# Performance work log

Hardware: AMD Instinct MI355X
Metric: run time of the kernel (lower is better)

## Reference

```python
import jax, jax.numpy as jnp
import numpy as np

N = 100000      # nodes
E = 1000000     # edges
IN = 128        # input features
H = 64          # hidden_channels
EPS = 1e-5      # BatchNorm eps


def _gcn_conv(x, W, b, src, dst, n):
    # PyG GCNConv: linear -> add self loops -> sym-norm -> scatter-add -> bias
    h = x @ W                                   # [n, H]
    loop = jnp.arange(n)
    s = jnp.concatenate([src, loop])            # [E+n]
    d = jnp.concatenate([dst, loop])
    deg = jax.ops.segment_sum(jnp.ones(s.shape, h.dtype), d, num_segments=n)
    dinv = jnp.where(deg > 0, jax.lax.rsqrt(deg), 0.0)
    norm = dinv[s] * dinv[d]                    # [E+n]
    out = jax.ops.segment_sum(h[s] * norm[:, None], d, num_segments=n)
    return out + b


def _bn_relu(x, gamma, beta):
    # BatchNorm1d, training-mode batch statistics (biased var), then ReLU
    m = x.mean(axis=0)
    v = x.var(axis=0)
    return jax.nn.relu((x - m) * jax.lax.rsqrt(v + EPS) * gamma + beta)


def setup_inputs() -> dict:
    key = jax.random.key(0)
    ks = jax.random.split(key, 10)
    x = jax.random.normal(ks[0], (N, IN), jnp.float32)
    edge_index = jax.random.randint(ks[1], (2, E), 0, N)
    W1 = jax.random.normal(ks[2], (IN, H), jnp.float32) / np.sqrt(IN)
    b1 = jnp.zeros((H,), jnp.float32)
    g1 = jnp.ones((H,), jnp.float32)
    bt1 = jnp.zeros((H,), jnp.float32)
    W2 = jax.random.normal(ks[3], (H, H), jnp.float32) / np.sqrt(H)
    b2 = jnp.zeros((H,), jnp.float32)
    g2 = jnp.ones((H,), jnp.float32)
    bt2 = jnp.zeros((H,), jnp.float32)
    return {"x": x, "edge_index": edge_index, "W1": W1, "b1": b1,
            "g1": g1, "bt1": bt1, "W2": W2, "b2": b2, "g2": g2, "bt2": bt2}


def reference(x, edge_index, W1, b1, g1, bt1, W2, b2, g2, bt2):
    src, dst = edge_index[0], edge_index[1]
    n = x.shape[0]
    h = _gcn_conv(x, W1, b1, src, dst, n)
    h = _bn_relu(h, g1, bt1)          # dropout omitted (deterministic reference)
    h = _gcn_conv(h, W2, b2, src, dst, n)
    h = _bn_relu(h, g2, bt2)
    return h
```

## Files before the change

### kernel.cpp

```cpp
#include <hip/hip_runtime.h>


#define IN_F 128
#define HID  64
#define SLOTS 64
static constexpr float BN_EPS = 1e-5f;

typedef float f32x4 __attribute__((ext_vector_type(4)));
typedef short bf16x8 __attribute__((ext_vector_type(8)));

__device__ inline unsigned short f2bf(float f) {
    union { float f; unsigned u; } v; v.f = f;
    unsigned r = v.u + 0x7FFFu + ((v.u >> 16) & 1u);
    return (unsigned short)(r >> 16);
}
__device__ inline float bf2f(unsigned short h) {
    union { unsigned u; float f; } v; v.u = (unsigned)h << 16;
    return v.f;
}


__global__ void fill_slots_convw(const int* __restrict__ src, const int* __restrict__ dst,
                                 int* __restrict__ cnt, int* __restrict__ slots, int E,
                                 const float* __restrict__ W1, const float* __restrict__ W2,
                                 unsigned short* __restrict__ W1t, unsigned short* __restrict__ W2t) {
    if (blockIdx.x == gridDim.x - 1) {
        int t = threadIdx.x;
        for (int i = t; i < HID * IN_F; i += 256) {
            int c = i >> 7, k = i & 127;
            W1t[i] = f2bf(W1[k * HID + c]);
        }
        for (int i = t; i < HID * HID; i += 256) {
            int c = i >> 6, k = i & 63;
            W2t[i] = f2bf(W2[k * HID + c]);
        }
        return;
    }
    int e = blockIdx.x * blockDim.x + threadIdx.x;
    if (e < E) {
        int d = dst[e];
        int pos = atomicAdd(&cnt[d], 1);
        if (pos < SLOTS) slots[(size_t)d * SLOTS + pos] = src[e];
    }
}


template <int K>
__global__ __launch_bounds__(256) void mfma_gemm_x(
    const float* __restrict__ X, const unsigned short* __restrict__ Wt,
    const int* __restrict__ cnt, unsigned short* __restrict__ out, int n) {
    constexpr int KS = K / 32;
    int t = threadIdx.x;
    int lane = t & 63, l15 = lane & 15, lhi = lane >> 4;
    bf16x8 Bf[4][KS];
#pragma unroll
    for (int cb = 0; cb < 4; ++cb)
#pragma unroll
        for (int ks = 0; ks < KS; ++ks)
            Bf[cb][ks] = *(const bf16x8*)&Wt[(cb * 16 + l15) * K + ks * 32 + lhi * 8];

    int wid = blockIdx.x * 4 + (t >> 6);
    int ntiles = n >> 4;
    if (wid >= ntiles) return;
    int r0 = wid << 4;
    const float* xrow = X + (size_t)(r0 + l15) * K;
    bf16x8 Af[KS];
#pragma unroll
    for (int ks = 0; ks < KS; ++ks) {
        float4 u = *(const float4*)&xrow[ks * 32 + lhi * 8];
        float4 v = *(const float4*)&xrow[ks * 32 + lhi * 8 + 4];
        bf16x8 a;
        a[0] = f2bf(u.x); a[1] = f2bf(u.y); a[2] = f2bf(u.z); a[3] = f2bf(u.w);
        a[4] = f2bf(v.x); a[5] = f2bf(v.y); a[6] = f2bf(v.z); a[7] = f2bf(v.w);
        Af[ks] = a;
    }
    f32x4 acc[4] = {{0.f,0.f,0.f,0.f},{0.f,0.f,0.f,0.f},{0.f,0.f,0.f,0.f},{0.f,0.f,0.f,0.f}};
#pragma unroll
    for (int cb = 0; cb < 4; ++cb)
#pragma unroll
        for (int ks = 0; ks < KS; ++ks)
            acc[cb] = __builtin_amdgcn_mfma_f32_16x16x32_bf16(Af[ks], Bf[cb][ks], acc[cb], 0, 0, 0);
#pragma unroll
    for (int j = 0; j < 4; ++j) {
        int r = r0 + lhi * 4 + j;
        float dv = rsqrtf((float)cnt[r] + 1.0f);
#pragma unroll
        for (int cb = 0; cb < 4; ++cb)
            out[(size_t)r * HID + cb * 16 + l15] = f2bf(acc[cb][j] * dv);
    }
}

__global__ __launch_bounds__(256) void mfma_gemm_bn(
    const unsigned short* __restrict__ V, const float* __restrict__ stats,
    const float* __restrict__ g, const float* __restrict__ beta,
    const unsigned short* __restrict__ Wt, const int* __restrict__ cnt,
    unsigned short* __restrict__ out, int n) {
    int t = threadIdx.x;
    int lane = t & 63, l15 = lane & 15, lhi = lane >> 4;
    bf16x8 Bf[4][2];
#pragma unroll
    for (int cb = 0; cb < 4; ++cb)
#pragma unroll
        for (int ks = 0; ks < 2; ++ks)
            Bf[cb][ks] = *(const bf16x8*)&Wt[(cb * 16 + l15) * HID + ks * 32 + lhi * 8];

    float aK[2][8], bK[2][8];
    float inv_n = 1.0f / (float)n;
#pragma unroll
    for (int ks = 0; ks < 2; ++ks)
#pragma unroll
        for (int e = 0; e < 8; ++e) {
            int k = ks * 32 + lhi * 8 + e;
            float m = stats[k] * inv_n;
            float var = stats[HID + k] * inv_n - m * m;
            float a = g[k] * rsqrtf(var + BN_EPS);
            aK[ks][e] = a;
            bK[ks][e] = beta[k] - m * a;
        }

    int wid = blockIdx.x * 4 + (t >> 6);
    int ntiles = n >> 4;
    if (wid >= ntiles) return;
    int r0 = wid << 4;
    const unsigned short* vrow = V + (size_t)(r0 + l15) * HID;
    bf16x8 Af[2];
#pragma unroll
    for (int ks = 0; ks < 2; ++ks) {
        bf16x8 raw = *(const bf16x8*)&vrow[ks * 32 + lhi * 8];
        bf16x8 a;
#pragma unroll
        for (int e = 0; e < 8; ++e) {
            float y = bf2f((unsigned short)raw[e]);
            a[e] = f2bf(fmaxf(fmaf(y, aK[ks][e], bK[ks][e]), 0.0f));
        }
        Af[ks] = a;
    }
    f32x4 acc[4] = {{0.f,0.f,0.f,0.f},{0.f,0.f,0.f,0.f},{0.f,0.f,0.f,0.f},{0.f,0.f,0.f,0.f}};
#pragma unroll
    for (int cb = 0; cb < 4; ++cb)
#pragma unroll
        for (int ks = 0; ks < 2; ++ks)
            acc[cb] = __builtin_amdgcn_mfma_f32_16x16x32_bf16(Af[ks], Bf[cb][ks], acc[cb], 0, 0, 0);
#pragma unroll
    for (int j = 0; j < 4; ++j) {
        int r = r0 + lhi * 4 + j;
        float dv = rsqrtf((float)cnt[r] + 1.0f);
#pragma unroll
        for (int cb = 0; cb < 4; ++cb)
            out[(size_t)r * HID + cb * 16 + l15] = f2bf(acc[cb][j] * dv);
    }
}


__global__ __launch_bounds__(256) void aggregate_stats_bf(
    const unsigned short* __restrict__ hs, const int* __restrict__ cntA,
    const int* __restrict__ slots, unsigned short* __restrict__ agg,
    float* __restrict__ stats, int n) {
    int t = threadIdx.x;
    int l16 = t & 15;
    int grp = (blockIdx.x * blockDim.x + t) >> 4;
    int ngrp = (gridDim.x * blockDim.x) >> 4;
    float st0 = 0.f, st1 = 0.f, st2 = 0.f, st3 = 0.f;
    float sq0 = 0.f, sq1 = 0.f, sq2 = 0.f, sq3 = 0.f;
    for (int i = grp; i < n; i += ngrp) {
        ushort4 sv = *(const ushort4*)&hs[(size_t)i * HID + 4 * l16];
        float acc[4][4] = {};
        acc[0][0] = bf2f(sv.x); acc[0][1] = bf2f(sv.y);
        acc[0][2] = bf2f(sv.z); acc[0][3] = bf2f(sv.w);
        int cnt = min(cntA[i], SLOTS);
        const int* b = slots + (size_t)i * SLOTS;
        int k = 0;
        while (k < cnt) {
            int take = min(cnt - k, 16);
            int idx = (l16 < take) ? b[k + l16] : 0;
            int j = 0;
            for (; j + 4 <= take; j += 4) {
                ushort4 vv[4];
#pragma unroll
                for (int u = 0; u < 4; ++u) {
                    int sI = __shfl(idx, j + u, 16);
                    vv[u] = *(const ushort4*)&hs[(size_t)sI * HID + 4 * l16];
                }
#pragma unroll
                for (int u = 0; u < 4; ++u) {
                    acc[u][0] += bf2f(vv[u].x); acc[u][1] += bf2f(vv[u].y);
                    acc[u][2] += bf2f(vv[u].z); acc[u][3] += bf2f(vv[u].w);
                }
            }
            for (; j < take; ++j) {
                int sI = __shfl(idx, j, 16);
                ushort4 vv = *(const ushort4*)&hs[(size_t)sI * HID + 4 * l16];
                acc[0][0] += bf2f(vv.x); acc[0][1] += bf2f(vv.y);
                acc[0][2] += bf2f(vv.z); acc[0][3] += bf2f(vv.w);
            }
            k += take;
        }
        float di = rsqrtf((float)cnt + 1.0f);
        float o0 = (acc[0][0] + acc[1][0] + acc[2][0] + acc[3][0]) * di;
        float o1 = (acc[0][1] + acc[1][1] + acc[2][1] + acc[3][1]) * di;
        float o2 = (acc[0][2] + acc[1][2] + acc[2][2] + acc[3][2]) * di;
        float o3 = (acc[0][3] + acc[1][3] + acc[2][3] + acc[3][3]) * di;
        ushort4 ov;
        ov.x = f2bf(o0); ov.y = f2bf(o1); ov.z = f2bf(o2); ov.w = f2bf(o3);
        *(ushort4*)&agg[(size_t)i * HID + 4 * l16] = ov;
        st0 += o0; st1 += o1; st2 += o2; st3 += o3;
        sq0 += o0 * o0; sq1 += o1 * o1; sq2 += o2 * o2; sq3 += o3 * o3;
    }
    __shared__ float ls[16][HID];
    __shared__ float ls2[16][HID];
    int gb = t >> 4;
    ls[gb][4 * l16 + 0] = st0; ls[gb][4 * l16 + 1] = st1;
    ls[gb][4 * l16 + 2] = st2; ls[gb][4 * l16 + 3] = st3;
    ls2[gb][4 * l16 + 0] = sq0; ls2[gb][4 * l16 + 1] = sq1;
    ls2[gb][4 * l16 + 2] = sq2; ls2[gb][4 * l16 + 3] = sq3;
    __syncthreads();
    if (t < HID) {
        float ts = 0.f, t2 = 0.f;
#pragma unroll
        for (int q = 0; q < 16; ++q) { ts += ls[q][t]; t2 += ls2[q][t]; }
        atomicAdd(&stats[t], ts);
        atomicAdd(&stats[HID + t], t2);
    }
}

__global__ void bn_apply_relu_bf(const unsigned short* __restrict__ v,
                                 const float* __restrict__ stats,
                                 const float* __restrict__ g, const float* __restrict__ beta,
                                 float* __restrict__ out, int n) {
    int i = blockIdx.x * blockDim.x + threadIdx.x;
    if (i >= n * (HID / 4)) return;
    int c4 = (i & 15) << 2;
    float inv_n = 1.0f / (float)n;
    ushort4 vv = ((const ushort4*)v)[i];
    float xs[4] = {bf2f(vv.x), bf2f(vv.y), bf2f(vv.z), bf2f(vv.w)};
    float o[4];
#pragma unroll
    for (int j = 0; j < 4; ++j) {
        int c = c4 + j;
        float m = stats[c] * inv_n;
        float var = stats[HID + c] * inv_n - m * m;
        float a = g[c] * rsqrtf(var + BN_EPS);
        float y = (xs[j] - m) * a + beta[c];
        o[j] = y > 0.0f ? y : 0.0f;
    }
    ((float4*)out)[i] = make_float4(o[0], o[1], o[2], o[3]);
}


extern "C" void kernel_launch(void* const* d_in, const int* in_sizes, int n_in,
                              void* d_out, int out_size, void* d_ws, size_t ws_size,
                              hipStream_t stream) {
    const float* x   = (const float*)d_in[0];
    const int*   ei  = (const int*)d_in[1];
    const float* W1  = (const float*)d_in[2];
    const float* g1  = (const float*)d_in[4];
    const float* bt1 = (const float*)d_in[5];
    const float* W2  = (const float*)d_in[6];
    const float* g2  = (const float*)d_in[8];
    const float* bt2 = (const float*)d_in[9];

    const int n = in_sizes[0] / IN_F;
    const int E = in_sizes[1] / 2;
    const int* src = ei;
    const int* dst = ei + E;

    char* w = (char*)d_ws;
    int*            cnt   = (int*)w;            w += (size_t)n * 4;
    float*          stats = (float*)w;          w += 256 * 4;
    unsigned short* W1t   = (unsigned short*)w; w += (size_t)HID * IN_F * 2;
    unsigned short* W2t   = (unsigned short*)w; w += (size_t)HID * HID * 2;
    int*            slots = (int*)w;            w += (size_t)n * SLOTS * 4;
    unsigned short* hs    = (unsigned short*)w; w += (size_t)n * HID * 2;
    unsigned short* aggB  = (unsigned short*)w;

    hipMemsetAsync(cnt, 0, (size_t)n * 4, stream);
    hipMemsetAsync(stats, 0, 256 * 4, stream);

    fill_slots_convw<<<(E + 255) / 256 + 1, 256, 0, stream>>>(src, dst, cnt, slots, E,
                                                              W1, W2, W1t, W2t);

    const int ntiles = n >> 4;
    const int gblk = (ntiles + 3) / 4;

    mfma_gemm_x<IN_F><<<gblk, 256, 0, stream>>>(x, W1t, cnt, hs, n);
    aggregate_stats_bf<<<2048, 256, 0, stream>>>(hs, cnt, slots, aggB, stats, n);

    mfma_gemm_bn<<<gblk, 256, 0, stream>>>(aggB, stats, g1, bt1, W2t, cnt, hs, n);
    aggregate_stats_bf<<<2048, 256, 0, stream>>>(hs, cnt, slots, aggB, stats + 128, n);
    bn_apply_relu_bf<<<(n * (HID / 4) + 255) / 256, 256, 0, stream>>>(
        aggB, stats + 128, g2, bt2, (float*)d_out, n);
}
```

Baseline: 349.6 us.

## Fuse edge-slot filling with first GEMM and move degree scaling into aggregation

The first GEMM no longer depends on the degree counts. Its output is left unscaled, and its blocks are interleaved 2:5 with edge-bucketing blocks in one launch so compute-bound MFMA work overlaps with atomic scatter work. A small kernel precomputes per-node dinv. The first aggregation then applies the source-node scaling per neighbor, using a dinv value gathered once per lane and broadcast by shuffle. This adds a per-edge dinv gather and extra FMAs in layer 1, plus two small extra launches (weight convert, make_dinv).

After: 335.2 us. -4.1%, faster.

```diff
diff --git a/kernel.cpp b/kernel.cpp
--- a/kernel.cpp
+++ b/kernel.cpp
@@ -20,80 +20,88 @@
 }
 
 
-__global__ void fill_slots_convw(const int* __restrict__ src, const int* __restrict__ dst,
-                                 int* __restrict__ cnt, int* __restrict__ slots, int E,
-                                 const float* __restrict__ W1, const float* __restrict__ W2,
-                                 unsigned short* __restrict__ W1t, unsigned short* __restrict__ W2t) {
-    if (blockIdx.x == gridDim.x - 1) {
+__global__ void convert_w(const float* __restrict__ W1, const float* __restrict__ W2,
+                          unsigned short* __restrict__ W1t, unsigned short* __restrict__ W2t) {
+    int t = threadIdx.x;
+    for (int i = t; i < HID * IN_F; i += 256) {
+        int c = i >> 7, k = i & 127;
+        W1t[i] = f2bf(W1[k * HID + c]);
+    }
+    for (int i = t; i < HID * HID; i += 256) {
+        int c = i >> 6, k = i & 63;
+        W2t[i] = f2bf(W2[k * HID + c]);
+    }
+}
+
+
+__global__ __launch_bounds__(256) void fused_fill_gemm1(
+    const float* __restrict__ X, const unsigned short* __restrict__ Wt,
+    const int* __restrict__ src, const int* __restrict__ dst,
+    int* __restrict__ cnt, int* __restrict__ slots, int E,
+    unsigned short* __restrict__ out, int n, int G, int F) {
+    int p = blockIdx.x / 7, r = blockIdx.x % 7;
+    if (r < 2) {
+        int gb = p * 2 + r;
+        if (gb >= G) return;
+        constexpr int K = IN_F, KS = K / 32;
         int t = threadIdx.x;
-        for (int i = t; i < HID * IN_F; i += 256) {
-            int c = i >> 7, k = i & 127;
-            W1t[i] = f2bf(W1[k * HID + c]);
-        }
-        for (int i = t; i < HID * HID; i += 256) {
-            int c = i >> 6, k = i & 63;
-            W2t[i] = f2bf(W2[k * HID + c]);
-        }
-        return;
-    }
-    int e = blockIdx.x * blockDim.x + threadIdx.x;
-    if (e < E) {
-        int d = dst[e];
-        int pos = atomicAdd(&cnt[d], 1);
-        if (pos < SLOTS) slots[(size_t)d * SLOTS + pos] = src[e];
-    }
-}
-
-
-template <int K>
-__global__ __launch_bounds__(256) void mfma_gemm_x(
-    const float* __restrict__ X, const unsigned short* __restrict__ Wt,
-    const int* __restrict__ cnt, unsigned short* __restrict__ out, int n) {
-    constexpr int KS = K / 32;
-    int t = threadIdx.x;
-    int lane = t & 63, l15 = lane & 15, lhi = lane >> 4;
-    bf16x8 Bf[4][KS];
-#pragma unroll
-    for (int cb = 0; cb < 4; ++cb)
-#pragma unroll
-        for (int ks = 0; ks < KS; ++ks)
-            Bf[cb][ks] = *(const bf16x8*)&Wt[(cb * 16 + l15) * K + ks * 32 + lhi * 8];
-
-    int wid = blockIdx.x * 4 + (t >> 6);
-    int ntiles = n >> 4;
-    if (wid >= ntiles) return;
-    int r0 = wid << 4;
-    const float* xrow = X + (size_t)(r0 + l15) * K;
-    bf16x8 Af[KS];
-#pragma unroll
-    for (int ks = 0; ks < KS; ++ks) {
-        float4 u = *(const float4*)&xrow[ks * 32 + lhi * 8];
-        float4 v = *(const float4*)&xrow[ks * 32 + lhi * 8 + 4];
-        bf16x8 a;
-        a[0] = f2bf(u.x); a[1] = f2bf(u.y); a[2] = f2bf(u.z); a[3] = f2bf(u.w);
-        a[4] = f2bf(v.x); a[5] = f2bf(v.y); a[6] = f2bf(v.z); a[7] = f2bf(v.w);
-        Af[ks] = a;
-    }
-    f32x4 acc[4] = {{0.f,0.f,0.f,0.f},{0.f,0.f,0.f,0.f},{0.f,0.f,0.f,0.f},{0.f,0.f,0.f,0.f}};
-#pragma unroll
-    for (int cb = 0; cb < 4; ++cb)
-#pragma unroll
-        for (int ks = 0; ks < KS; ++ks)
-            acc[cb] = __builtin_amdgcn_mfma_f32_16x16x32_bf16(Af[ks], Bf[cb][ks], acc[cb], 0, 0, 0);
-#pragma unroll
-    for (int j = 0; j < 4; ++j) {
-        int r = r0 + lhi * 4 + j;
-        float dv = rsqrtf((float)cnt[r] + 1.0f);
+        int lane = t & 63, l15 = lane & 15, lhi = lane >> 4;
+        bf16x8 Bf[4][KS];
 #pragma unroll
         for (int cb = 0; cb < 4; ++cb)
-            out[(size_t)r * HID + cb * 16 + l15] = f2bf(acc[cb][j] * dv);
-    }
-}
+#pragma unroll
+            for (int ks = 0; ks < KS; ++ks)
+                Bf[cb][ks] = *(const bf16x8*)&Wt[(cb * 16 + l15) * K + ks * 32 + lhi * 8];
+        int wid = gb * 4 + (t >> 6);
+        int ntiles = n >> 4;
+        if (wid >= ntiles) return;
+        int r0 = wid << 4;
+        const float* xrow = X + (size_t)(r0 + l15) * K;
+        bf16x8 Af[KS];
+#pragma unroll
+        for (int ks = 0; ks < KS; ++ks) {
+            float4 u = *(const float4*)&xrow[ks * 32 + lhi * 8];
+            float4 v = *(const float4*)&xrow[ks * 32 + lhi * 8 + 4];
+            bf16x8 a;
+            a[0] = f2bf(u.x); a[1] = f2bf(u.y); a[2] = f2bf(u.z); a[3] = f2bf(u.w);
+            a[4] = f2bf(v.x); a[5] = f2bf(v.y); a[6] = f2bf(v.z); a[7] = f2bf(v.w);
+            Af[ks] = a;
+        }
+        f32x4 acc[4] = {{0.f,0.f,0.f,0.f},{0.f,0.f,0.f,0.f},{0.f,0.f,0.f,0.f},{0.f,0.f,0.f,0.f}};
+#pragma unroll
+        for (int cb = 0; cb < 4; ++cb)
+#pragma unroll
+            for (int ks = 0; ks < KS; ++ks)
+                acc[cb] = __builtin_amdgcn_mfma_f32_16x16x32_bf16(Af[ks], Bf[cb][ks], acc[cb], 0, 0, 0);
+#pragma unroll
+        for (int j = 0; j < 4; ++j) {
+            int rr = r0 + lhi * 4 + j;
+#pragma unroll
+            for (int cb = 0; cb < 4; ++cb)
+                out[(size_t)rr * HID + cb * 16 + l15] = f2bf(acc[cb][j]);
+        }
+    } else {
+        int fb = p * 5 + (r - 2);
+        if (fb >= F) return;
+        int e = fb * 256 + threadIdx.x;
+        if (e < E) {
+            int d = dst[e];
+            int pos = atomicAdd(&cnt[d], 1);
+            if (pos < SLOTS) slots[(size_t)d * SLOTS + pos] = src[e];
+        }
+    }
+}
+
+__global__ void make_dinv(const int* __restrict__ cnt, float* __restrict__ dinvF, int n) {
+    int i = blockIdx.x * blockDim.x + threadIdx.x;
+    if (i < n) dinvF[i] = rsqrtf((float)cnt[i] + 1.0f);
+}
+
 
 __global__ __launch_bounds__(256) void mfma_gemm_bn(
     const unsigned short* __restrict__ V, const float* __restrict__ stats,
     const float* __restrict__ g, const float* __restrict__ beta,
-    const unsigned short* __restrict__ Wt, const int* __restrict__ cnt,
+    const unsigned short* __restrict__ Wt, const float* __restrict__ dinvF,
     unsigned short* __restrict__ out, int n) {
     int t = threadIdx.x;
     int lane = t & 63, l15 = lane & 15, lhi = lane >> 4;
@@ -144,7 +152,7 @@
 #pragma unroll
     for (int j = 0; j < 4; ++j) {
         int r = r0 + lhi * 4 + j;
-        float dv = rsqrtf((float)cnt[r] + 1.0f);
+        float dv = dinvF[r];
 #pragma unroll
         for (int cb = 0; cb < 4; ++cb)
             out[(size_t)r * HID + cb * 16 + l15] = f2bf(acc[cb][j] * dv);
@@ -152,10 +160,11 @@
 }
 
 
+template <bool PRESCALED>
 __global__ __launch_bounds__(256) void aggregate_stats_bf(
     const unsigned short* __restrict__ hs, const int* __restrict__ cntA,
-    const int* __restrict__ slots, unsigned short* __restrict__ agg,
-    float* __restrict__ stats, int n) {
+    const float* __restrict__ dinvF, const int* __restrict__ slots,
+    unsigned short* __restrict__ agg, float* __restrict__ stats, int n) {
     int t = threadIdx.x;
     int l16 = t & 15;
     int grp = (blockIdx.x * blockDim.x + t) >> 4;
@@ -163,39 +172,55 @@
     float st0 = 0.f, st1 = 0.f, st2 = 0.f, st3 = 0.f;
     float sq0 = 0.f, sq1 = 0.f, sq2 = 0.f, sq3 = 0.f;
     for (int i = grp; i < n; i += ngrp) {
+        float di = dinvF[i];
         ushort4 sv = *(const ushort4*)&hs[(size_t)i * HID + 4 * l16];
+        float selfs = PRESCALED ? 1.0f : di;
         float acc[4][4] = {};
-        acc[0][0] = bf2f(sv.x); acc[0][1] = bf2f(sv.y);
-        acc[0][2] = bf2f(sv.z); acc[0][3] = bf2f(sv.w);
+        acc[0][0] = bf2f(sv.x) * selfs; acc[0][1] = bf2f(sv.y) * selfs;
+        acc[0][2] = bf2f(sv.z) * selfs; acc[0][3] = bf2f(sv.w) * selfs;
         int cnt = min(cntA[i], SLOTS);
         const int* b = slots + (size_t)i * SLOTS;
         int k = 0;
         while (k < cnt) {
             int take = min(cnt - k, 16);
-            int idx = (l16 < take) ? b[k + l16] : 0;
+            int idx = 0; float dvl = 0.f;
+            if (l16 < take) {
+                idx = b[k + l16];
+                if (!PRESCALED) dvl = dinvF[idx];
+            }
             int j = 0;
             for (; j + 4 <= take; j += 4) {
-                ushort4 vv[4];
+                ushort4 vv[4]; float dv4[4];
 #pragma unroll
                 for (int u = 0; u < 4; ++u) {
                     int sI = __shfl(idx, j + u, 16);
+                    if (!PRESCALED) dv4[u] = __shfl(dvl, j + u, 16);
                     vv[u] = *(const ushort4*)&hs[(size_t)sI * HID + 4 * l16];
                 }
 #pragma unroll
                 for (int u = 0; u < 4; ++u) {
-                    acc[u][0] += bf2f(vv[u].x); acc[u][1] += bf2f(vv[u].y);
-                    acc[u][2] += bf2f(vv[u].z); acc[u][3] += bf2f(vv[u].w);
+                    if (PRESCALED) {
+                        acc[u][0] += bf2f(vv[u].x); acc[u][1] += bf2f(vv[u].y);
+                        acc[u][2] += bf2f(vv[u].z); acc[u][3] += bf2f(vv[u].w);
+                    } else {
+                        acc[u][0] = fmaf(bf2f(vv[u].x), dv4[u], acc[u][0]);
+                        acc[u][1] = fmaf(bf2f(vv[u].y), dv4[u], acc[u][1]);
+                        acc[u][2] = fmaf(bf2f(vv[u].z), dv4[u], acc[u][2]);
+                        acc[u][3] = fmaf(bf2f(vv[u].w), dv4[u], acc[u][3]);
+                    }
                 }
             }
             for (; j < take; ++j) {
                 int sI = __shfl(idx, j, 16);
+                float dv1 = PRESCALED ? 1.0f : __shfl(dvl, j, 16);
                 ushort4 vv = *(const ushort4*)&hs[(size_t)sI * HID + 4 * l16];
-                acc[0][0] += bf2f(vv.x); acc[0][1] += bf2f(vv.y);
-                acc[0][2] += bf2f(vv.z); acc[0][3] += bf2f(vv.w);
+                acc[0][0] = fmaf(bf2f(vv.x), dv1, acc[0][0]);
+                acc[0][1] = fmaf(bf2f(vv.y), dv1, acc[0][1]);
+                acc[0][2] = fmaf(bf2f(vv.z), dv1, acc[0][2]);
+                acc[0][3] = fmaf(bf2f(vv.w), dv1, acc[0][3]);
             }
             k += take;
         }
-        float di = rsqrtf((float)cnt + 1.0f);
         float o0 = (acc[0][0] + acc[1][0] + acc[2][0] + acc[3][0]) * di;
         float o1 = (acc[0][1] + acc[1][1] + acc[2][1] + acc[3][1]) * di;
         float o2 = (acc[0][2] + acc[1][2] + acc[2][2] + acc[3][2]) * di;
@@ -266,6 +291,7 @@
 
     char* w = (char*)d_ws;
     int*            cnt   = (int*)w;            w += (size_t)n * 4;
+    float*          dinvF = (float*)w;          w += (size_t)n * 4;
     float*          stats = (float*)w;          w += 256 * 4;
     unsigned short* W1t   = (unsigned short*)w; w += (size_t)HID * IN_F * 2;
     unsigned short* W2t   = (unsigned short*)w; w += (size_t)HID * HID * 2;
@@ -276,17 +302,20 @@
     hipMemsetAsync(cnt, 0, (size_t)n * 4, stream);
     hipMemsetAsync(stats, 0, 256 * 4, stream);
 
-    fill_slots_convw<<<(E + 255) / 256 + 1, 256, 0, stream>>>(src, dst, cnt, slots, E,
-                                                              W1, W2, W1t, W2t);
+    convert_w<<<1, 256, 0, stream>>>(W1, W2, W1t, W2t);
 
     const int ntiles = n >> 4;
-    const int gblk = (ntiles + 3) / 4;
-
-    mfma_gemm_x<IN_F><<<gblk, 256, 0, stream>>>(x, W1t, cnt, hs, n);
-    aggregate_stats_bf<<<2048, 256, 0, stream>>>(hs, cnt, slots, aggB, stats, n);
-
-    mfma_gemm_bn<<<gblk, 256, 0, stream>>>(aggB, stats, g1, bt1, W2t, cnt, hs, n);
-    aggregate_stats_bf<<<2048, 256, 0, stream>>>(hs, cnt, slots, aggB, stats + 128, n);
+    const int G = (ntiles + 3) / 4;
+    const int F = (E + 255) / 256;
+    const int periods = (((G + 1) / 2) > ((F + 4) / 5)) ? ((G + 1) / 2) : ((F + 4) / 5);
+    fused_fill_gemm1<<<periods * 7, 256, 0, stream>>>(x, W1t, src, dst, cnt, slots, E,
+                                                      hs, n, G, F);
+    make_dinv<<<(n + 255) / 256, 256, 0, stream>>>(cnt, dinvF, n);
+
+    aggregate_stats_bf<false><<<2048, 256, 0, stream>>>(hs, cnt, dinvF, slots, aggB, stats, n);
+
+    mfma_gemm_bn<<<G, 256, 0, stream>>>(aggB, stats, g1, bt1, W2t, dinvF, hs, n);
+    aggregate_stats_bf<true><<<2048, 256, 0, stream>>>(hs, cnt, dinvF, slots, aggB, stats + 128, n);
     bn_apply_relu_bf<<<(n * (HID / 4) + 255) / 256, 256, 0, stream>>>(
         aggB, stats + 128, g2, bt2, (float*)d_out, n);
 }
```
